# Kernel tuning notes

Hardware: AMD Instinct MI355X
Metric: run time of the kernel (lower is better)

## Reference

```python
import jax, jax.numpy as jnp
import numpy as np

NEG = -1e30  # effective -inf, safe under logaddexp


def _rna_loss(logits, targets, fbank_len, text_len, blank=0):
    """RNA loss: forward lattice DP over (T, U).

    logits: [B, T, U, V] raw scores (U = max_labels + 1)
    targets: [B, U-1] int labels; fbank_len/text_len: [B] int lengths.
    Each frame emits exactly one symbol (blank -> stay at u, label -> u+1).
    """
    log_probs = jax.nn.log_softmax(logits, axis=-1)          # [B,T,U,V]
    B, T, U, V = logits.shape
    L = U - 1
    lab = targets.astype(jnp.int32)                          # [B,L]
    lp_blank = jnp.transpose(log_probs[..., blank], (1, 0, 2))   # [T,B,U]
    # prob of emitting label u+1 while at state u: gather target token
    lp_label = jnp.take_along_axis(
        log_probs[:, :, :L, :], lab[:, None, :, None], axis=3)[..., 0]  # [B,T,L]
    lp_label = jnp.transpose(lp_label, (1, 0, 2))            # [T,B,L]

    alpha0 = jnp.full((B, U), NEG, dtype=log_probs.dtype).at[:, 0].set(0.0)

    def step(alpha, xs):
        lpb, lpl = xs                                        # [B,U], [B,L]
        stay = alpha + lpb                                   # emit blank
        move = jnp.pad(alpha[:, :L] + lpl, ((0, 0), (1, 0)),
                       constant_values=NEG)                  # emit label
        new = jnp.logaddexp(stay, move)
        return new, new

    _, alphas = jax.lax.scan(step, alpha0, (lp_blank, lp_label))  # [T,B,U]
    alphas = jnp.concatenate([alpha0[None], alphas], axis=0)      # [T+1,B,U]
    ll = alphas[fbank_len, jnp.arange(B), text_len]               # [B]
    return -ll


def setup_inputs() -> dict:
    key = jax.random.key(0)
    k1, k2, k3, k4 = jax.random.split(key, 4)
    B, T, L, V = 4, 512, 64, 1024
    logits = jax.random.normal(k1, (B, T, L + 1, V), dtype=jnp.float32)
    targets = jax.random.randint(k2, (B, L), 1, V, dtype=jnp.int32)
    fbank_len = jax.random.randint(k3, (B,), 384, T + 1, dtype=jnp.int32)
    text_len = jax.random.randint(k4, (B,), 32, L + 1, dtype=jnp.int32)
    return {"logits": logits, "targets": targets,
            "fbank_len": fbank_len, "text_len": text_len}


def reference(logits, targets, fbank_len, text_len):
    loss = _rna_loss(logits, targets, fbank_len, text_len, blank=0)
    return loss.mean()  # reduction='mean'
```

## Files before the change

kernel.cpp:

```cpp
#include <hip/hip_runtime.h>

#define NEGF (-1e30f)

namespace {

constexpr int B = 4, T = 512, L = 64, U = 65, V = 1024;

__device__ __forceinline__ float lse2(float a, float b) {
    float m = fmaxf(a, b);
    float d = fminf(a, b) - m;
    return m + __logf(1.0f + __expf(d));
}

__device__ __forceinline__ float dpp_bcast_op_max(float x) {
    x = fmaxf(x, __int_as_float(__builtin_amdgcn_update_dpp(0, __float_as_int(x), 0xB1, 0xF, 0xF, true)));
    x = fmaxf(x, __int_as_float(__builtin_amdgcn_update_dpp(0, __float_as_int(x), 0x4E, 0xF, 0xF, true)));
    x = fmaxf(x, __int_as_float(__builtin_amdgcn_update_dpp(0, __float_as_int(x), 0x141, 0xF, 0xF, true)));
    x = fmaxf(x, __int_as_float(__builtin_amdgcn_update_dpp(0, __float_as_int(x), 0x140, 0xF, 0xF, true)));
    x = fmaxf(x, __shfl_xor(x, 16, 64));
    x = fmaxf(x, __shfl_xor(x, 32, 64));
    return x;
}
__device__ __forceinline__ float dpp_bcast_op_sum(float x) {
    x += __int_as_float(__builtin_amdgcn_update_dpp(0, __float_as_int(x), 0xB1, 0xF, 0xF, true));
    x += __int_as_float(__builtin_amdgcn_update_dpp(0, __float_as_int(x), 0x4E, 0xF, 0xF, true));
    x += __int_as_float(__builtin_amdgcn_update_dpp(0, __float_as_int(x), 0x141, 0xF, 0xF, true));
    x += __int_as_float(__builtin_amdgcn_update_dpp(0, __float_as_int(x), 0x140, 0xF, 0xF, true));
    x += __shfl_xor(x, 16, 64);
    x += __shfl_xor(x, 32, 64);
    return x;
}

__global__ __launch_bounds__(256) void rna_lse_kernel(
    const float* __restrict__ logits, const int* __restrict__ targets,
    const int* __restrict__ fbank_len, const int* __restrict__ text_len,
    float* __restrict__ lpb, float* __restrict__ lpl) {
    const int lane = threadIdx.x & 63;
    const int row  = blockIdx.x * 4 + (threadIdx.x >> 6);
    const int u  = row % U;
    const int bt = row / U;
    const int t  = bt % T;
    const int b  = bt / T;

    const int fb = fbank_len[b];
    const int tl = text_len[b];
    if (t >= fb || u > tl || u > t + 1 || (tl - u) > (fb - t)) return;

    const float*  p  = logits + (size_t)row * V;
    const float4* p4 = (const float4*)p;
    float4 v0 = p4[lane];
    float4 v1 = p4[lane + 64];
    float4 v2 = p4[lane + 128];
    float4 v3 = p4[lane + 192];

    float m = fmaxf(fmaxf(fmaxf(v0.x, v0.y), fmaxf(v0.z, v0.w)),
              fmaxf(fmaxf(fmaxf(v1.x, v1.y), fmaxf(v1.z, v1.w)),
              fmaxf(fmaxf(fmaxf(v2.x, v2.y), fmaxf(v2.z, v2.w)),
                    fmaxf(fmaxf(v3.x, v3.y), fmaxf(v3.z, v3.w)))));
    m = dpp_bcast_op_max(m);

    float s = __expf(v0.x - m) + __expf(v0.y - m) + __expf(v0.z - m) + __expf(v0.w - m)
            + __expf(v1.x - m) + __expf(v1.y - m) + __expf(v1.z - m) + __expf(v1.w - m)
            + __expf(v2.x - m) + __expf(v2.y - m) + __expf(v2.z - m) + __expf(v2.w - m)
            + __expf(v3.x - m) + __expf(v3.y - m) + __expf(v3.z - m) + __expf(v3.w - m);
    s = dpp_bcast_op_sum(s);

    if (lane == 0) {
        float lse = m + __logf(s);
        lpb[(b * U + u) * T + t] = v0.x - lse;
        if (u < L) {
            int tgt = targets[b * L + u];
            lpl[(b * U + u + 1) * T + t] = p[tgt] - lse;
        }
    }
}

__global__ __launch_bounds__(256, 1) void rna_dp_kernel(
    const float* __restrict__ lpb, const float* __restrict__ lpl,
    const int* __restrict__ fbank_len, const int* __restrict__ text_len,
    float* __restrict__ out) {
    __shared__ float res[B];
    const int lane = threadIdx.x & 63;
    const int b    = threadIdx.x >> 6;
    const int fb   = fbank_len[b];
    const int tl   = text_len[b];

    const float* pbR   = lpb + (b * U + lane) * T;
    const float* plR   = lpl + (b * U + lane) * T;
    const float* pbR64 = lpb + (b * U + 64) * T;
    const float* plR64 = lpl + (b * U + 64) * T;

    float alpha   = (lane == 0) ? 0.0f : NEGF;
    float alpha64 = NEGF;

    float cb[16], cl[16], cb64[16], cl64[16];
#pragma unroll
    for (int q = 0; q < 4; ++q) {
        float4 a = *(const float4*)(pbR   + 4 * q);
        float4 c = *(const float4*)(plR   + 4 * q);
        float4 e = *(const float4*)(pbR64 + 4 * q);
        float4 g = *(const float4*)(plR64 + 4 * q);
        cb[4*q+0]=a.x; cb[4*q+1]=a.y; cb[4*q+2]=a.z; cb[4*q+3]=a.w;
        cl[4*q+0]=c.x; cl[4*q+1]=c.y; cl[4*q+2]=c.z; cl[4*q+3]=c.w;
        cb64[4*q+0]=e.x; cb64[4*q+1]=e.y; cb64[4*q+2]=e.z; cb64[4*q+3]=e.w;
        cl64[4*q+0]=g.x; cl64[4*q+1]=g.y; cl64[4*q+2]=g.z; cl64[4*q+3]=g.w;
    }

    for (int t0 = 0; t0 < fb; t0 += 16) {
        float nb[16], nl[16], nb64[16], nl64[16];
        const bool pf = (t0 + 16 < fb);
        if (pf) {
            const int tn = t0 + 16;
#pragma unroll
            for (int q = 0; q < 4; ++q) {
                float4 a = *(const float4*)(pbR   + tn + 4 * q);
                float4 c = *(const float4*)(plR   + tn + 4 * q);
                float4 e = *(const float4*)(pbR64 + tn + 4 * q);
                float4 g = *(const float4*)(plR64 + tn + 4 * q);
                nb[4*q+0]=a.x; nb[4*q+1]=a.y; nb[4*q+2]=a.z; nb[4*q+3]=a.w;
                nl[4*q+0]=c.x; nl[4*q+1]=c.y; nl[4*q+2]=c.z; nl[4*q+3]=c.w;
                nb64[4*q+0]=e.x; nb64[4*q+1]=e.y; nb64[4*q+2]=e.z; nb64[4*q+3]=e.w;
                nl64[4*q+0]=g.x; nl64[4*q+1]=g.y; nl64[4*q+2]=g.z; nl64[4*q+3]=g.w;
            }
        }
#pragma unroll
        for (int j = 0; j < 16; ++j) {
            if (t0 + j >= fb) break;
            const int t = t0 + j;
            float ap = __int_as_float(__builtin_amdgcn_update_dpp(
                0, __float_as_int(alpha), 0x138, 0xF, 0xF, true));
            float stay = alpha + cb[j];
            float move = (lane == 0) ? NEGF : (ap + cl[j]);
            float na   = lse2(stay, move);
            float stay64 = alpha64 + cb64[j];
            float move64 = alpha + cl64[j];
            alpha64 = lse2(stay64, move64);
            alpha   = na;
            if (lane > t + 1) alpha = NEGF;
            if (t + 1 < 64)   alpha64 = NEGF;
        }
        if (pf) {
#pragma unroll
            for (int j = 0; j < 16; ++j) {
                cb[j] = nb[j]; cl[j] = nl[j]; cb64[j] = nb64[j]; cl64[j] = nl64[j];
            }
        }
    }

    float ans = (tl < 64) ? __shfl(alpha, tl, 64) : __shfl(alpha64, 63, 64);
    if (lane == 0) res[b] = ans;
    __syncthreads();
    if (threadIdx.x == 0)
        out[0] = -(res[0] + res[1] + res[2] + res[3]) * (1.0f / B);
}

}

extern "C" void kernel_launch(void* const* d_in, const int* in_sizes, int n_in,
                              void* d_out, int out_size, void* d_ws, size_t ws_size,
                              hipStream_t stream) {
    const float* logits  = (const float*)d_in[0];
    const int*   targets = (const int*)d_in[1];
    const int*   fbl     = (const int*)d_in[2];
    const int*   txl     = (const int*)d_in[3];
    float* lpb = (float*)d_ws;
    float* lpl = lpb + (size_t)B * U * T;
    float* out = (float*)d_out;

    const int rows = B * T * U;
    rna_lse_kernel<<<rows / 4, 256, 0, stream>>>(logits, targets, fbl, txl, lpb, lpl);
    rna_dp_kernel<<<1, 256, 0, stream>>>(lpb, lpl, fbl, txl, out);
}
```

Baseline: 707.9 us.

## Split DP across one workgroup per batch and widen the register prefetch chunk

The DP kernel now launches one 64-thread workgroup per batch element instead of a single 256-thread block, so each wave can run on its own CU. The per-iteration break check is replaced by whole chunks of 32 timesteps plus a scalar tail loop. A tiny third kernel sums the per-batch partial results. This is meant to cut scheduling contention and branch overhead in the serial DP, at the cost of an extra kernel launch and higher register pressure from the larger prefetch buffers.

```diff
diff --git a/kernel.cpp b/kernel.cpp
--- a/kernel.cpp
+++ b/kernel.cpp
@@ -29,6 +29,11 @@
     x += __shfl_xor(x, 16, 64);
     x += __shfl_xor(x, 32, 64);
     return x;
+}
+
+__device__ __forceinline__ float dpp_shr1(float x) {
+    return __int_as_float(__builtin_amdgcn_update_dpp(
+        0, __float_as_int(x), 0x138, 0xF, 0xF, true));
 }
 
 __global__ __launch_bounds__(256) void rna_lse_kernel(
@@ -75,13 +80,12 @@
     }
 }
 
-__global__ __launch_bounds__(256, 1) void rna_dp_kernel(
+__global__ __launch_bounds__(64, 1) void rna_dp_kernel(
     const float* __restrict__ lpb, const float* __restrict__ lpl,
     const int* __restrict__ fbank_len, const int* __restrict__ text_len,
-    float* __restrict__ out) {
-    __shared__ float res[B];
-    const int lane = threadIdx.x & 63;
-    const int b    = threadIdx.x >> 6;
+    float* __restrict__ partial) {
+    const int lane = threadIdx.x;
+    const int b    = blockIdx.x;
     const int fb   = fbank_len[b];
     const int tl   = text_len[b];
 
@@ -93,42 +97,43 @@
     float alpha   = (lane == 0) ? 0.0f : NEGF;
     float alpha64 = NEGF;
 
-    float cb[16], cl[16], cb64[16], cl64[16];
+    constexpr int G = 32;
+    float cb[G], cl[G], cb64[G], cl64[G];
 #pragma unroll
-    for (int q = 0; q < 4; ++q) {
-        float4 a = *(const float4*)(pbR   + 4 * q);
-        float4 c = *(const float4*)(plR   + 4 * q);
-        float4 e = *(const float4*)(pbR64 + 4 * q);
-        float4 g = *(const float4*)(plR64 + 4 * q);
-        cb[4*q+0]=a.x; cb[4*q+1]=a.y; cb[4*q+2]=a.z; cb[4*q+3]=a.w;
-        cl[4*q+0]=c.x; cl[4*q+1]=c.y; cl[4*q+2]=c.z; cl[4*q+3]=c.w;
-        cb64[4*q+0]=e.x; cb64[4*q+1]=e.y; cb64[4*q+2]=e.z; cb64[4*q+3]=e.w;
-        cl64[4*q+0]=g.x; cl64[4*q+1]=g.y; cl64[4*q+2]=g.z; cl64[4*q+3]=g.w;
+    for (int q = 0; q < G / 4; ++q) {
+        float4 a  = *(const float4*)(pbR   + 4 * q);
+        float4 c  = *(const float4*)(plR   + 4 * q);
+        float4 e  = *(const float4*)(pbR64 + 4 * q);
+        float4 g4 = *(const float4*)(plR64 + 4 * q);
+        cb[4*q+0]=a.x;  cb[4*q+1]=a.y;  cb[4*q+2]=a.z;  cb[4*q+3]=a.w;
+        cl[4*q+0]=c.x;  cl[4*q+1]=c.y;  cl[4*q+2]=c.z;  cl[4*q+3]=c.w;
+        cb64[4*q+0]=e.x;  cb64[4*q+1]=e.y;  cb64[4*q+2]=e.z;  cb64[4*q+3]=e.w;
+        cl64[4*q+0]=g4.x; cl64[4*q+1]=g4.y; cl64[4*q+2]=g4.z; cl64[4*q+3]=g4.w;
     }
 
-    for (int t0 = 0; t0 < fb; t0 += 16) {
-        float nb[16], nl[16], nb64[16], nl64[16];
-        const bool pf = (t0 + 16 < fb);
+    const int nFull = fb / G;
+    for (int g = 0; g < nFull; ++g) {
+        const int t0 = g * G;
+        float nb[G], nl[G], nb64[G], nl64[G];
+        const bool pf = (g + 1 < nFull);
         if (pf) {
-            const int tn = t0 + 16;
+            const int tn = t0 + G;
 #pragma unroll
-            for (int q = 0; q < 4; ++q) {
-                float4 a = *(const float4*)(pbR   + tn + 4 * q);
-                float4 c = *(const float4*)(plR   + tn + 4 * q);
-                float4 e = *(const float4*)(pbR64 + tn + 4 * q);
-                float4 g = *(const float4*)(plR64 + tn + 4 * q);
-                nb[4*q+0]=a.x; nb[4*q+1]=a.y; nb[4*q+2]=a.z; nb[4*q+3]=a.w;
-                nl[4*q+0]=c.x; nl[4*q+1]=c.y; nl[4*q+2]=c.z; nl[4*q+3]=c.w;
-                nb64[4*q+0]=e.x; nb64[4*q+1]=e.y; nb64[4*q+2]=e.z; nb64[4*q+3]=e.w;
-                nl64[4*q+0]=g.x; nl64[4*q+1]=g.y; nl64[4*q+2]=g.z; nl64[4*q+3]=g.w;
+            for (int q = 0; q < G / 4; ++q) {
+                float4 a  = *(const float4*)(pbR   + tn + 4 * q);
+                float4 c  = *(const float4*)(plR   + tn + 4 * q);
+                float4 e  = *(const float4*)(pbR64 + tn + 4 * q);
+                float4 g4 = *(const float4*)(plR64 + tn + 4 * q);
+                nb[4*q+0]=a.x;  nb[4*q+1]=a.y;  nb[4*q+2]=a.z;  nb[4*q+3]=a.w;
+                nl[4*q+0]=c.x;  nl[4*q+1]=c.y;  nl[4*q+2]=c.z;  nl[4*q+3]=c.w;
+                nb64[4*q+0]=e.x;  nb64[4*q+1]=e.y;  nb64[4*q+2]=e.z;  nb64[4*q+3]=e.w;
+                nl64[4*q+0]=g4.x; nl64[4*q+1]=g4.y; nl64[4*q+2]=g4.z; nl64[4*q+3]=g4.w;
             }
         }
 #pragma unroll
-        for (int j = 0; j < 16; ++j) {
-            if (t0 + j >= fb) break;
+        for (int j = 0; j < G; ++j) {
             const int t = t0 + j;
-            float ap = __int_as_float(__builtin_amdgcn_update_dpp(
-                0, __float_as_int(alpha), 0x138, 0xF, 0xF, true));
+            float ap   = dpp_shr1(alpha);
             float stay = alpha + cb[j];
             float move = (lane == 0) ? NEGF : (ap + cl[j]);
             float na   = lse2(stay, move);
@@ -141,17 +146,36 @@
         }
         if (pf) {
 #pragma unroll
-            for (int j = 0; j < 16; ++j) {
+            for (int j = 0; j < G; ++j) {
                 cb[j] = nb[j]; cl[j] = nl[j]; cb64[j] = nb64[j]; cl64[j] = nl64[j];
             }
         }
     }
 
+    for (int t = nFull * G; t < fb; ++t) {
+        float bj  = pbR[t];
+        float lj  = plR[t];
+        float b64 = pbR64[t];
+        float l64 = plR64[t];
+        float ap   = dpp_shr1(alpha);
+        float stay = alpha + bj;
+        float move = (lane == 0) ? NEGF : (ap + lj);
+        float na   = lse2(stay, move);
+        float stay64 = alpha64 + b64;
+        float move64 = alpha + l64;
+        alpha64 = lse2(stay64, move64);
+        alpha   = na;
+        if (lane > t + 1) alpha = NEGF;
+        if (t + 1 < 64)   alpha64 = NEGF;
+    }
+
     float ans = (tl < 64) ? __shfl(alpha, tl, 64) : __shfl(alpha64, 63, 64);
-    if (lane == 0) res[b] = ans;
-    __syncthreads();
-    if (threadIdx.x == 0)
-        out[0] = -(res[0] + res[1] + res[2] + res[3]) * (1.0f / B);
+    if (lane == 0) partial[b] = ans;
+}
+
+__global__ void rna_sum_kernel(const float* __restrict__ partial,
+                               float* __restrict__ out) {
+    out[0] = -(partial[0] + partial[1] + partial[2] + partial[3]) * (1.0f / B);
 }
 
 }
@@ -163,11 +187,13 @@
     const int*   targets = (const int*)d_in[1];
     const int*   fbl     = (const int*)d_in[2];
     const int*   txl     = (const int*)d_in[3];
-    float* lpb = (float*)d_ws;
-    float* lpl = lpb + (size_t)B * U * T;
-    float* out = (float*)d_out;
+    float* lpb     = (float*)d_ws;
+    float* lpl     = lpb + (size_t)B * U * T;
+    float* partial = lpl + (size_t)B * U * T;
+    float* out     = (float*)d_out;
 
     const int rows = B * T * U;
     rna_lse_kernel<<<rows / 4, 256, 0, stream>>>(logits, targets, fbl, txl, lpb, lpl);
-    rna_dp_kernel<<<1, 256, 0, stream>>>(lpb, lpl, fbl, txl, out);
+    rna_dp_kernel<<<B, 64, 0, stream>>>(lpb, lpl, fbl, txl, partial);
+    rna_sum_kernel<<<1, 1, 0, stream>>>(partial, out);
 }
```

Measured after the change: 717.5 us. About the same (+1.4%).
